# Kernel optimization log

Measured on AMD Instinct MI355X. Metric: run time of the kernel, lower is better.

Reference implementation:

```python
import jax, jax.numpy as jnp
import numpy as np

EPS = 1e-12  # matches torch F.normalize eps


def _l2n(x, axis):
    return x / jnp.maximum(jnp.linalg.norm(x, axis=axis, keepdims=True), EPS)


def setup_inputs() -> dict:
    key = jax.random.key(0)
    k1, k2, k3 = jax.random.split(key, 3)
    x = jax.random.normal(k1, (4, 128, 30, 40), dtype=jnp.float32)
    conv_w = jax.random.normal(k2, (64, 128), dtype=jnp.float32) * 0.02  # 1x1 conv, no bias (vladv2=False)
    centroids = jax.random.uniform(k3, (64, 128), dtype=jnp.float32)
    return {"x": x, "conv_w": conv_w, "centroids": centroids}


def reference(x, conv_w, centroids):
    N, C, H, W = x.shape
    K = centroids.shape[0]
    ps, stride = 4, 1  # patch_sizes='4', strides='1'

    # descriptor-wise L2 normalization of input
    x = _l2n(x, 1)

    # 1x1 conv + softmax over clusters -> soft assignment [N,K,H,W]
    soft_assign = jax.nn.softmax(jnp.einsum('kc,nchw->nkhw', conv_w, x), axis=1)

    # weighted residuals [N,K,C,H,W] (vectorized form of the per-cluster loop)
    res = (x[:, None] - centroids[None, :, :, None, None]) * soft_assign[:, :, None]

    # global VLAD: sum over spatial, intra-norm, flatten, L2-norm
    vlad_global = res.sum(axis=(-1, -2))            # [N,K,C]
    vlad_global = _l2n(vlad_global, 2).reshape(N, K * C)
    vlad_global = _l2n(vlad_global, 1)

    # integral image over spatial dims with zero pad on top/left
    r = res.reshape(N, K * C, H, W)
    integ = jnp.cumsum(jnp.cumsum(r, axis=-1), axis=-2)
    integ = jnp.pad(integ, ((0, 0), (0, 0), (1, 0), (1, 0)))  # [N,KC,H+1,W+1]

    # dilated 2x2 box-filter conv == 4-corner integral-image lookup
    TL = integ[:, :, :H + 1 - ps:stride, :W + 1 - ps:stride]
    TR = integ[:, :, :H + 1 - ps:stride, ps::stride]
    BL = integ[:, :, ps::stride, :W + 1 - ps:stride]
    BR = integ[:, :, ps::stride, ps::stride]
    vl = (TL - TR - BL + BR) / (ps * ps)            # [N,KC,Hp,Wp]
    Hp, Wp = vl.shape[-2], vl.shape[-1]

    # local VLAD: intra-norm over descriptor dim, then global L2 per patch
    vl = vl.reshape(N, K, C, Hp * Wp)
    vl = _l2n(vl, 2).reshape(N, K * C, Hp * Wp)
    vlad_local = _l2n(vl, 1)

    return vlad_global, vlad_local
```

## Files before the change

### kernel.cpp

```cpp
#include <hip/hip_runtime.h>
#include <math.h>

#define EPSV 1e-12f

namespace {
constexpr int N_  = 4;
constexpr int C_  = 128;
constexpr int H_  = 30;
constexpr int W_  = 40;
constexpr int K_  = 64;
constexpr int HW_ = H_ * W_;
constexpr int HP_ = 27;
constexpr int WP_ = 37;
constexpr int P_  = HP_ * WP_;
constexpr int PS_ = 1000;
constexpr int KC_ = K_ * C_;
constexpr int CP_ = C_ * P_;
constexpr int CS_ = HP_ * W_;
constexpr int SL_ = CS_ / 4;
constexpr int CVP_ = 132;
}

static __device__ __forceinline__ float4 ld4(const float* p) {
    return *reinterpret_cast<const float4*>(p);
}
static __device__ __forceinline__ float dot4(float4 a, float4 b) {
    return a.x * b.x + a.y * b.y + a.z * b.z + a.w * b.w;
}
static __device__ __forceinline__ float4 f4add(float4 a, float4 b) {
    return make_float4(a.x + b.x, a.y + b.y, a.z + b.z, a.w + b.w);
}

__global__ __launch_bounds__(256) void k1_norm_softmax(
    const float* __restrict__ x, const float* __restrict__ conv_w,
    float* __restrict__ xnT, float* __restrict__ xnP, float* __restrict__ sa)
{
    __shared__ float xrow[C_ * W_];
    __shared__ float conv_s[K_ * CVP_];
    __shared__ float xrowT[W_ * CVP_];
    __shared__ float invn[W_];
    __shared__ float s_s[K_ * W_];

    const int b = blockIdx.x;
    const int n = b / H_, h = b - n * H_;
    const int t = threadIdx.x;

    for (int i = t; i < C_ * W_; i += 256) {
        const int c = i / W_, w = i - c * W_;
        xrow[i] = x[(size_t)(n * C_ + c) * HW_ + h * W_ + w];
    }
    for (int i = t; i < K_ * C_; i += 256) {
        const int k = i >> 7, c = i & 127;
        conv_s[k * CVP_ + c] = conv_w[i];
    }
    __syncthreads();

    if (t < W_) {
        float s = 0.f;
        for (int c = 0; c < C_; ++c) { const float v = xrow[c * W_ + t]; s += v * v; }
        invn[t] = 1.f / fmaxf(sqrtf(s), EPSV);
    }
    __syncthreads();

    for (int i = t; i < C_ * W_; i += 256) {
        const int c = i / W_, w = i - c * W_;
        const float v = xrow[i] * invn[w];
        xrow[i] = v;
        xnT[(size_t)(n * C_ + c) * HW_ + h * W_ + w] = v;
    }
    __syncthreads();

    for (int i = t; i < W_ * C_; i += 256) {
        const int w = i / C_, c = i - w * C_;
        const float v = xrow[c * W_ + w];
        xnP[((size_t)n * HW_ + h * W_ + w) * C_ + c] = v;
        xrowT[w * CVP_ + c] = v;
    }
    __syncthreads();

    {
        const int k = t >> 2, q = t & 3;
        float acc0 = 0.f, acc1 = 0.f, acc2 = 0.f, acc3 = 0.f, acc4 = 0.f;
        float acc5 = 0.f, acc6 = 0.f, acc7 = 0.f, acc8 = 0.f, acc9 = 0.f;
        const float* convk = &conv_s[k * CVP_];
        for (int ch = 0; ch < 4; ++ch) {
            float4 cv0 = ld4(convk + ch * 32 + 0),  cv1 = ld4(convk + ch * 32 + 4);
            float4 cv2 = ld4(convk + ch * 32 + 8),  cv3 = ld4(convk + ch * 32 + 12);
            float4 cv4 = ld4(convk + ch * 32 + 16), cv5 = ld4(convk + ch * 32 + 20);
            float4 cv6 = ld4(convk + ch * 32 + 24), cv7 = ld4(convk + ch * 32 + 28);
#pragma unroll
            for (int wi = 0; wi < 10; ++wi) {
                const float* xw = &xrowT[(q * 10 + wi) * CVP_ + ch * 32];
                float s = dot4(cv0, ld4(xw)) + dot4(cv1, ld4(xw + 4))
                        + dot4(cv2, ld4(xw + 8)) + dot4(cv3, ld4(xw + 12))
                        + dot4(cv4, ld4(xw + 16)) + dot4(cv5, ld4(xw + 20))
                        + dot4(cv6, ld4(xw + 24)) + dot4(cv7, ld4(xw + 28));
                if      (wi == 0) acc0 += s; else if (wi == 1) acc1 += s;
                else if (wi == 2) acc2 += s; else if (wi == 3) acc3 += s;
                else if (wi == 4) acc4 += s; else if (wi == 5) acc5 += s;
                else if (wi == 6) acc6 += s; else if (wi == 7) acc7 += s;
                else if (wi == 8) acc8 += s; else              acc9 += s;
            }
        }
        float* sd = &s_s[k * W_ + q * 10];
        sd[0] = acc0; sd[1] = acc1; sd[2] = acc2; sd[3] = acc3; sd[4] = acc4;
        sd[5] = acc5; sd[6] = acc6; sd[7] = acc7; sd[8] = acc8; sd[9] = acc9;
    }
    __syncthreads();

    if (t < W_) {
        const int w = t;
        float m = -1e30f;
        for (int k = 0; k < K_; ++k) m = fmaxf(m, s_s[k * W_ + w]);
        float sum = 0.f;
        for (int k = 0; k < K_; ++k) sum += expf(s_s[k * W_ + w] - m);
        const float inv = 1.f / sum;
        for (int k = 0; k < K_; ++k)
            sa[(size_t)(n * K_ + k) * HW_ + h * W_ + w] = expf(s_s[k * W_ + w] - m) * inv;
    }
}

#define COLSUM_VEC_T(cs_q, sa_s, x0, x1, x2, x3)                                \
    for (int s = t; s < SL_; s += 256) {                                        \
        const int i = s * 4;                                                    \
        const float4 sa0 = ld4(&sa_s[i]);                                       \
        const float4 sa1 = ld4(&sa_s[i + W_]);                                  \
        const float4 sa2 = ld4(&sa_s[i + 2 * W_]);                              \
        const float4 sa3 = ld4(&sa_s[i + 3 * W_]);                              \
        float acc[4][4];                                                        \
        const float* xc[4] = {x0, x1, x2, x3};                                  \
        _Pragma("unroll")                                                       \
        for (int ch = 0; ch < 4; ++ch) {                                        \
            const float4 a0 = ld4(xc[ch] + i);                                  \
            const float4 a1 = ld4(xc[ch] + i + W_);                             \
            const float4 a2 = ld4(xc[ch] + i + 2 * W_);                         \
            const float4 a3 = ld4(xc[ch] + i + 3 * W_);                         \
            acc[0][ch] = sa0.x * a0.x + sa1.x * a1.x + sa2.x * a2.x + sa3.x * a3.x; \
            acc[1][ch] = sa0.y * a0.y + sa1.y * a1.y + sa2.y * a2.y + sa3.y * a3.y; \
            acc[2][ch] = sa0.z * a0.z + sa1.z * a1.z + sa2.z * a2.z + sa3.z * a3.z; \
            acc[3][ch] = sa0.w * a0.w + sa1.w * a1.w + sa2.w * a2.w + sa3.w * a3.w; \
        }                                                                       \
        _Pragma("unroll")                                                       \
        for (int q = 0; q < 4; ++q)                                             \
            cs_q[q][s] = make_float4(acc[q][0], acc[q][1], acc[q][2], acc[q][3]); \
    }

#define WINDOW10(cs_q, b0, d, A0, A1, A2, A3)                                   \
    {                                                                           \
        float4 v0 = cs_q[(b0 + 0) & 3][(b0 + 0) >> 2];                          \
        float4 v1 = cs_q[(b0 + 1) & 3][(b0 + 1) >> 2];                          \
        float4 v2 = cs_q[(b0 + 2) & 3][(b0 + 2) >> 2];                          \
        float4 v3 = cs_q[(b0 + 3) & 3][(b0 + 3) >> 2];                          \
        float4 v4 = cs_q[(b0 + 4) & 3][(b0 + 4) >> 2];                          \
        float4 v5 = cs_q[(b0 + 5) & 3][(b0 + 5) >> 2];                          \
        float4 v6 = cs_q[(b0 + 6) & 3][(b0 + 6) >> 2];                          \
        float4 v7 = cs_q[(b0 + 7) & 3][(b0 + 7) >> 2];                          \
        float4 v8 = cs_q[(b0 + 8) & 3][(b0 + 8) >> 2];                          \
        float4 v9 = cs_q[(b0 + 9) & 3][(b0 + 9) >> 2];                          \
        const float4 t0 = f4add(v0, v1), t1 = f4add(v1, v2), t2 = f4add(v2, v3);\
        const float4 t3 = f4add(v3, v4), t4 = f4add(v4, v5), t5 = f4add(v5, v6);\
        const float4 t6 = f4add(v6, v7), t7 = f4add(v7, v8), t8 = f4add(v8, v9);\
        const float4 w0 = f4add(t0, t2), w1 = f4add(t1, t3), w2 = f4add(t2, t4);\
        const float4 w3 = f4add(t3, t5), w4 = f4add(t4, t6), w5 = f4add(t5, t7);\
        const float4 w6 = f4add(t6, t8);                                        \
        A0 = (0 < d) ? w0 : w3;                                                 \
        A1 = (1 < d) ? w1 : w4;                                                 \
        A2 = (2 < d) ? w2 : w5;                                                 \
        A3 = (3 < d) ? w3 : w6;                                                 \
    }

__global__ __launch_bounds__(256) void k4_merged(
    const float* __restrict__ sa, const float* __restrict__ xnT,
    const float* __restrict__ xnP, const float* __restrict__ cent,
    float* __restrict__ nsqp, float* __restrict__ vg_u,
    float* __restrict__ vg_r)
{
    __shared__ float  sa_s[HW_ + 8];
    __shared__ float4 cs_q[4][SL_ + 1];
    __shared__ float  gs[256], bss[256];
    __shared__ float  red[2];

    const int t = threadIdx.x;

    if (blockIdx.x < 256) {
        const int b = blockIdx.x;
        const int n = b >> 6, k = b & 63;
        const int c = t & 127, half = t >> 7;
        constexpr int HHW = HW_ / 2;

        const float* sarow = &sa[(size_t)b * HW_ + half * HHW];
        const float* xp = &xnP[((size_t)n * HW_ + half * HHW) * C_ + c];
        float g0 = 0.f, g1 = 0.f, g2 = 0.f, g3 = 0.f;
        float b0 = 0.f, b1 = 0.f, b2 = 0.f, b3 = 0.f;
        for (int pix = 0; pix < HHW; pix += 4) {
            const float s0 = sarow[pix + 0], s1 = sarow[pix + 1];
            const float s2 = sarow[pix + 2], s3 = sarow[pix + 3];
            g0 += s0 * xp[(size_t)(pix + 0) * C_];
            g1 += s1 * xp[(size_t)(pix + 1) * C_];
            g2 += s2 * xp[(size_t)(pix + 2) * C_];
            g3 += s3 * xp[(size_t)(pix + 3) * C_];
            b0 += s0; b1 += s1; b2 += s2; b3 += s3;
        }
        gs[t]  = (g0 + g1) + (g2 + g3);
        bss[t] = (b0 + b1) + (b2 + b3);
        __syncthreads();

        float vg = 0.f;
        if (t < 128) {
            vg = (gs[t] + gs[t + 128]) - cent[k * C_ + c] * (bss[t] + bss[t + 128]);
            float nsq = vg * vg;
            for (int off = 32; off >= 1; off >>= 1) nsq += __shfl_down(nsq, off);
            if ((t & 63) == 0) red[t >> 6] = nsq;
        }
        __syncthreads();
        const float tot  = red[0] + red[1];
        const float norm = sqrtf(tot);
        const float iv   = 1.f / fmaxf(norm, EPSV);
        if (t < 128) vg_u[(size_t)b * C_ + t] = vg * iv;
        if (t == 0) { const float rr = norm * iv; vg_r[b] = rr * rr; }
        return;
    }

    const int b  = blockIdx.x - 256;
    const int cq = b & 3;
    const int nk = b >> 2;
    const int n  = nk >> 6, k = nk & 63;

    for (int i = t; i < HW_; i += 256) sa_s[i] = sa[(size_t)nk * HW_ + i];
    __syncthreads();

    int hp0 = 0, b0 = 0, d = 4;
    float B0 = 0.f, B1 = 0.f, B2 = 0.f, B3 = 0.f;
    if (t < 250) {
        const int p0 = 4 * t;
        hp0 = p0 / WP_;
        const int wp0 = p0 - hp0 * WP_;
        b0 = p0 + 3 * hp0;
        d  = WP_ - wp0;
        const float* r0 = &sa_s[hp0 * W_ + wp0];
        float sc[10];
#pragma unroll
        for (int j = 0; j < 10; ++j)
            sc[j] = r0[j] + r0[j + W_] + r0[j + 2 * W_] + r0[j + 3 * W_];
        const float u0 = sc[0] + sc[1], u1 = sc[1] + sc[2], u2 = sc[2] + sc[3];
        const float u3 = sc[3] + sc[4], u4 = sc[4] + sc[5], u5 = sc[5] + sc[6];
        const float u6 = sc[6] + sc[7], u7 = sc[7] + sc[8], u8 = sc[8] + sc[9];
        const float wB0 = u0 + u2, wB1 = u1 + u3, wB2 = u2 + u4;
        const float wB3 = u3 + u5, wB4 = u4 + u6, wB5 = u5 + u7, wB6 = u6 + u8;
        B0 = (0 < d) ? wB0 : wB3;
        B1 = (1 < d) ? wB1 : wB4;
        B2 = (2 < d) ? wB2 : wB5;
        B3 = (3 < d) ? wB3 : wB6;
    }

    float4 nv0 = make_float4(0, 0, 0, 0), nv1 = nv0, nv2 = nv0, nv3 = nv0;
    const float* xb = xnT + (size_t)n * C_ * HW_;

    for (int g = 0; g < 8; ++g) {
        const int c0 = cq * 32 + g * 4;
        const float* x0 = xb + (size_t)(c0 + 0) * HW_;
        const float* x1 = xb + (size_t)(c0 + 1) * HW_;
        const float* x2 = xb + (size_t)(c0 + 2) * HW_;
        const float* x3 = xb + (size_t)(c0 + 3) * HW_;
        __syncthreads();
        COLSUM_VEC_T(cs_q, sa_s, x0, x1, x2, x3)
        __syncthreads();
        if (t < 250) {
            const float4 ce = ld4(&cent[k * C_ + c0]);
            float4 A0, A1, A2, A3;
            WINDOW10(cs_q, b0, d, A0, A1, A2, A3)
            const float4 e0 = make_float4(A0.x - ce.x * B0, A0.y - ce.y * B0,
                                          A0.z - ce.z * B0, A0.w - ce.w * B0);
            const float4 e1 = make_float4(A1.x - ce.x * B1, A1.y - ce.y * B1,
                                          A1.z - ce.z * B1, A1.w - ce.w * B1);
            const float4 e2 = make_float4(A2.x - ce.x * B2, A2.y - ce.y * B2,
                                          A2.z - ce.z * B2, A2.w - ce.w * B2);
            const float4 e3 = make_float4(A3.x - ce.x * B3, A3.y - ce.y * B3,
                                          A3.z - ce.z * B3, A3.w - ce.w * B3);
            nv0 = make_float4(nv0.x + e0.x * e0.x, nv0.y + e0.y * e0.y,
                              nv0.z + e0.z * e0.z, nv0.w + e0.w * e0.w);
            nv1 = make_float4(nv1.x + e1.x * e1.x, nv1.y + e1.y * e1.y,
                              nv1.z + e1.z * e1.z, nv1.w + e1.w * e1.w);
            nv2 = make_float4(nv2.x + e2.x * e2.x, nv2.y + e2.y * e2.y,
                              nv2.z + e2.z * e2.z, nv2.w + e2.w * e2.w);
            nv3 = make_float4(nv3.x + e3.x * e3.x, nv3.y + e3.y * e3.y,
                              nv3.z + e3.z * e3.z, nv3.w + e3.w * e3.w);
        }
    }
    if (t < 250) {
        const float s0 = (nv0.x + nv0.y) + (nv0.z + nv0.w);
        const float s1 = (nv1.x + nv1.y) + (nv1.z + nv1.w);
        const float s2 = (nv2.x + nv2.y) + (nv2.z + nv2.w);
        const float s3 = (nv3.x + nv3.y) + (nv3.z + nv3.w);
        *reinterpret_cast<float4*>(&nsqp[(size_t)b * PS_ + 4 * t]) =
            make_float4(s0 * 0.00390625f, s1 * 0.00390625f,
                        s2 * 0.00390625f, s3 * 0.00390625f);
    }
}

__global__ __launch_bounds__(256) void k5_merged(
    const float* __restrict__ nsqp, float* __restrict__ inv1,
    float* __restrict__ rloc, const float* __restrict__ vg_u,
    const float* __restrict__ vg_r, float* __restrict__ out)
{
    const int t = threadIdx.x;
    if (blockIdx.x >= 256) {
        const int n = blockIdx.x - 256;
        __shared__ float inv2s;
        if (t == 0) {
            float s = 0.f;
            for (int k = 0; k < K_; ++k) s += vg_r[n * K_ + k];
            inv2s = 1.f / fmaxf(sqrtf(s), EPSV);
        }
        __syncthreads();
        const float inv2 = inv2s;
        for (int i = t; i < KC_; i += 256)
            out[(size_t)n * KC_ + i] = vg_u[(size_t)n * KC_ + i] * inv2;
        return;
    }
    const int nk = blockIdx.x;
    if (t < 250) {
        const int p0 = 4 * t;
        const float4 a = ld4(&nsqp[(size_t)(nk * 4 + 0) * PS_ + p0]);
        const float4 b = ld4(&nsqp[(size_t)(nk * 4 + 1) * PS_ + p0]);
        const float4 c = ld4(&nsqp[(size_t)(nk * 4 + 2) * PS_ + p0]);
        const float4 e = ld4(&nsqp[(size_t)(nk * 4 + 3) * PS_ + p0]);
        float4 iv, rr;
#pragma unroll
        for (int j = 0; j < 4; ++j) {
            const float s = reinterpret_cast<const float*>(&a)[j]
                          + reinterpret_cast<const float*>(&b)[j]
                          + reinterpret_cast<const float*>(&c)[j]
                          + reinterpret_cast<const float*>(&e)[j];
            const float norm = sqrtf(s);
            const float v = 1.f / fmaxf(norm, EPSV);
            reinterpret_cast<float*>(&iv)[j] = v * 0.0625f;
            const float r = norm * v;
            reinterpret_cast<float*>(&rr)[j] = r * r;
        }
        *reinterpret_cast<float4*>(&inv1[(size_t)nk * PS_ + p0]) = iv;
        *reinterpret_cast<float4*>(&rloc[(size_t)nk * PS_ + p0]) = rr;
    }
}

__global__ __launch_bounds__(256) void k6_inv2(
    const float* __restrict__ rloc, float* __restrict__ inv2)
{
    const int n = blockIdx.x;
    const int t = threadIdx.x;
    if (t < 250) {
        const int p0 = 4 * t;
        float4 s = make_float4(0, 0, 0, 0);
        for (int k = 0; k < K_; ++k) {
            const float4 r = ld4(&rloc[(size_t)(n * K_ + k) * PS_ + p0]);
            s = f4add(s, r);
        }
        float4 o;
        o.x = 1.f / fmaxf(sqrtf(s.x), EPSV);
        o.y = 1.f / fmaxf(sqrtf(s.y), EPSV);
        o.z = 1.f / fmaxf(sqrtf(s.z), EPSV);
        o.w = 1.f / fmaxf(sqrtf(s.w), EPSV);
        *reinterpret_cast<float4*>(&inv2[n * PS_ + p0]) = o;
    }
}

__global__ __launch_bounds__(256) void k7_write(
    const float* __restrict__ sa, const float* __restrict__ xnT,
    const float* __restrict__ cent, const float* __restrict__ inv1,
    const float* __restrict__ inv2, float* __restrict__ outl)
{
    __shared__ float  sa_s[HW_ + 8];
    __shared__ float  scl_s[P_];
    __shared__ float  t2_s[P_];
    __shared__ float4 cs_q[4][SL_ + 1];

    const int b  = blockIdx.x;
    const int cq = b & 3;
    const int nk = b >> 2;
    const int n  = nk >> 6, k = nk & 63;
    const int t  = threadIdx.x;

    for (int i = t; i < HW_; i += 256) sa_s[i] = sa[(size_t)nk * HW_ + i];
    __syncthreads();
    for (int p = t; p < P_; p += 256) {
        const int hp = p / WP_, wp = p - hp * WP_;
        float bs = 0.f;
#pragma unroll
        for (int dh = 0; dh < 4; ++dh) {
            const float* r = &sa_s[(hp + dh) * W_ + wp];
            bs += r[0] + r[1] + r[2] + r[3];
        }
        const float sc = inv1[(size_t)nk * PS_ + p] * inv2[n * PS_ + p];
        scl_s[p] = sc;
        t2_s[p]  = bs * sc;
    }

    const float* xb = xnT + (size_t)n * C_ * HW_;
    float* ob = outl + (size_t)nk * CP_;

    for (int g = 0; g < 8; ++g) {
        const int m = g & 3, h8 = g >> 2;
        const int c0 = cq * 32 + h8 * 16 + m;
        const float* x0 = xb + (size_t)(c0 + 0) * HW_;
        const float* x1 = xb + (size_t)(c0 + 4) * HW_;
        const float* x2 = xb + (size_t)(c0 + 8) * HW_;
        const float* x3 = xb + (size_t)(c0 + 12) * HW_;
        __syncthreads();
        COLSUM_VEC_T(cs_q, sa_s, x0, x1, x2, x3)
        __syncthreads();
        const float ce0 = cent[k * C_ + c0];
        const float ce1 = cent[k * C_ + c0 + 4];
        const float ce2 = cent[k * C_ + c0 + 8];
        const float ce3 = cent[k * C_ + c0 + 12];
        float* ob0 = ob + (size_t)(c0 + 0) * P_;
        float* ob1 = ob + (size_t)(c0 + 4) * P_;
        float* ob2 = ob + (size_t)(c0 + 8) * P_;
        float* ob3 = ob + (size_t)(c0 + 12) * P_;

        if (t < 249) {
            const int p0 = m + 4 * t;
            const int hp0 = p0 / WP_;
            const int wp0 = p0 - hp0 * WP_;
            const int b0 = p0 + 3 * hp0;
            const int d  = WP_ - wp0;
            const float sc0 = scl_s[p0 + 0], sc1 = scl_s[p0 + 1];
            const float sc2 = scl_s[p0 + 2], sc3 = scl_s[p0 + 3];
            const float tt0 = t2_s[p0 + 0], tt1 = t2_s[p0 + 1];
            const float tt2 = t2_s[p0 + 2], tt3 = t2_s[p0 + 3];
            float4 A0, A1, A2, A3;
            WINDOW10(cs_q, b0, d, A0, A1, A2, A3)
            const float4 s0v = make_float4(A0.x * sc0 - ce0 * tt0, A1.x * sc1 - ce0 * tt1,
                                           A2.x * sc2 - ce0 * tt2, A3.x * sc3 - ce0 * tt3);
            const float4 s1v = make_float4(A0.y * sc0 - ce1 * tt0, A1.y * sc1 - ce1 * tt1,
                                           A2.y * sc2 - ce1 * tt2, A3.y * sc3 - ce1 * tt3);
            const float4 s2v = make_float4(A0.z * sc0 - ce2 * tt0, A1.z * sc1 - ce2 * tt1,
                                           A2.z * sc2 - ce2 * tt2, A3.z * sc3 - ce2 * tt3);
            const float4 s3v = make_float4(A0.w * sc0 - ce3 * tt0, A1.w * sc1 - ce3 * tt1,
                                           A2.w * sc2 - ce3 * tt2, A3.w * sc3 - ce3 * tt3);
            *reinterpret_cast<float4*>(ob0 + p0) = s0v;
            *reinterpret_cast<float4*>(ob1 + p0) = s1v;
            *reinterpret_cast<float4*>(ob2 + p0) = s2v;
            *reinterpret_cast<float4*>(ob3 + p0) = s3v;
        } else if (t < 252) {
            const int u = t - 249;
            const int p = (u < m) ? u : 996 + u;
            const int hp = p / WP_, wp = p - hp * WP_;
            const int base = hp * W_ + wp;
            const float4 s0 = cs_q[(base + 0) & 3][(base + 0) >> 2];
            const float4 s1 = cs_q[(base + 1) & 3][(base + 1) >> 2];
            const float4 s2 = cs_q[(base + 2) & 3][(base + 2) >> 2];
            const float4 s3 = cs_q[(base + 3) & 3][(base + 3) >> 2];
            const float sc = scl_s[p], tt = t2_s[p];
            ob0[p] = (s0.x + s1.x + s2.x + s3.x) * sc - ce0 * tt;
            ob1[p] = (s0.y + s1.y + s2.y + s3.y) * sc - ce1 * tt;
            ob2[p] = (s0.z + s1.z + s2.z + s3.z) * sc - ce2 * tt;
            ob3[p] = (s0.w + s1.w + s2.w + s3.w) * sc - ce3 * tt;
        }
    }
}

extern "C" void kernel_launch(void* const* d_in, const int* in_sizes, int n_in,
                              void* d_out, int out_size, void* d_ws, size_t ws_size,
                              hipStream_t stream)
{
    const float* x      = (const float*)d_in[0];
    const float* conv_w = (const float*)d_in[1];
    const float* cent   = (const float*)d_in[2];
    float* out = (float*)d_out;
    float* ws  = (float*)d_ws;

    float* xnT  = ws;
    float* xnP  = ws + 614400;
    float* sa   = ws + 1228800;
    float* vg_u = ws + 1536000;
    float* vg_r = ws + 1568768;
    float* nsqp = ws + 1569024;
    float* inv1 = ws + 2593024;
    float* rloc = ws + 2849024;
    float* inv2 = ws + 3105024;

    float* outl = out + (size_t)N_ * KC_;

    k1_norm_softmax<<<N_ * H_, 256, 0, stream>>>(x, conv_w, xnT, xnP, sa);
    k4_merged<<<256 + N_ * K_ * 4, 256, 0, stream>>>(sa, xnT, xnP, cent,
                                                     nsqp, vg_u, vg_r);
    k5_merged<<<256 + N_, 256, 0, stream>>>(nsqp, inv1, rloc, vg_u, vg_r, out);
    k6_inv2<<<N_, 256, 0, stream>>>(rloc, inv2);
    k7_write<<<N_ * K_ * 4, 256, 0, stream>>>(sa, xnT, cent, inv1, inv2, outl);
}
```

Measured before the change: 120.2 us.

## Compute column sums with vertical strip reuse and process 8 channels per pass

Replaces the per-row 4-tap column-sum loop with a strip scheme. Each thread loads 7 rows of a 4-wide column once and forms four overlapping vertical 4-sums, so loaded rows and softmax weights are reused instead of reloaded. The column-sum buffer is doubled so each iteration handles 8 channels instead of 4, halving the number of barrier-separated passes in both the norm and output kernels. The cost is that only 140 of 256 threads compute column sums, register pressure rises from the 28 float4 partials, and shared memory use grows.

New measurement: 118.9 us. No clear change (-1.0%).

```diff
diff --git a/kernel.cpp b/kernel.cpp
--- a/kernel.cpp
+++ b/kernel.cpp
@@ -29,6 +29,9 @@
 }
 static __device__ __forceinline__ float4 f4add(float4 a, float4 b) {
     return make_float4(a.x + b.x, a.y + b.y, a.z + b.z, a.w + b.w);
+}
+static __device__ __forceinline__ float4 f4mul(float4 a, float4 b) {
+    return make_float4(a.x * b.x, a.y * b.y, a.z * b.z, a.w * b.w);
 }
 
 __global__ __launch_bounds__(256) void k1_norm_softmax(
@@ -120,43 +123,55 @@
     }
 }
 
-#define COLSUM_VEC_T(cs_q, sa_s, x0, x1, x2, x3)                                \
-    for (int s = t; s < SL_; s += 256) {                                        \
-        const int i = s * 4;                                                    \
-        const float4 sa0 = ld4(&sa_s[i]);                                       \
-        const float4 sa1 = ld4(&sa_s[i + W_]);                                  \
-        const float4 sa2 = ld4(&sa_s[i + 2 * W_]);                              \
-        const float4 sa3 = ld4(&sa_s[i + 3 * W_]);                              \
-        float acc[4][4];                                                        \
-        const float* xc[4] = {x0, x1, x2, x3};                                  \
+#define COLSUM_STRIP(cs_q, sa_s, xb, cA_base)                                   \
+    if (t < 140) {                                                              \
+        const int q2 = t / 70, item = t - q2 * 70;                              \
+        const int hq = item / 10, wq = item - hq * 10;                          \
+        const int h0 = 4 * hq;                                                  \
+        const int nh = (hq < 6) ? 4 : 3;                                        \
+        const int cA = (cA_base) + q2 * 16;                                     \
+        const float* xp0 = xb + (size_t)(cA + 0)  * HW_ + h0 * W_ + 4 * wq;     \
+        const float* xp1 = xb + (size_t)(cA + 4)  * HW_ + h0 * W_ + 4 * wq;     \
+        const float* xp2 = xb + (size_t)(cA + 8)  * HW_ + h0 * W_ + 4 * wq;     \
+        const float* xp3 = xb + (size_t)(cA + 12) * HW_ + h0 * W_ + 4 * wq;     \
+        const float* sap = &sa_s[h0 * W_ + 4 * wq];                             \
+        float4 p0[7], p1[7], p2[7], p3[7];                                      \
         _Pragma("unroll")                                                       \
-        for (int ch = 0; ch < 4; ++ch) {                                        \
-            const float4 a0 = ld4(xc[ch] + i);                                  \
-            const float4 a1 = ld4(xc[ch] + i + W_);                             \
-            const float4 a2 = ld4(xc[ch] + i + 2 * W_);                         \
-            const float4 a3 = ld4(xc[ch] + i + 3 * W_);                         \
-            acc[0][ch] = sa0.x * a0.x + sa1.x * a1.x + sa2.x * a2.x + sa3.x * a3.x; \
-            acc[1][ch] = sa0.y * a0.y + sa1.y * a1.y + sa2.y * a2.y + sa3.y * a3.y; \
-            acc[2][ch] = sa0.z * a0.z + sa1.z * a1.z + sa2.z * a2.z + sa3.z * a3.z; \
-            acc[3][ch] = sa0.w * a0.w + sa1.w * a1.w + sa2.w * a2.w + sa3.w * a3.w; \
+        for (int r = 0; r < 7; ++r) {                                           \
+            const float4 sv = ld4(sap + r * W_);                                \
+            p0[r] = f4mul(sv, ld4(xp0 + r * W_));                               \
+            p1[r] = f4mul(sv, ld4(xp1 + r * W_));                               \
+            p2[r] = f4mul(sv, ld4(xp2 + r * W_));                               \
+            p3[r] = f4mul(sv, ld4(xp3 + r * W_));                               \
         }                                                                       \
         _Pragma("unroll")                                                       \
-        for (int q = 0; q < 4; ++q)                                             \
-            cs_q[q][s] = make_float4(acc[q][0], acc[q][1], acc[q][2], acc[q][3]); \
-    }
-
-#define WINDOW10(cs_q, b0, d, A0, A1, A2, A3)                                   \
+        for (int hh = 0; hh < 4; ++hh) {                                        \
+            if (hh < nh) {                                                      \
+                const float4 c0v = f4add(f4add(p0[hh], p0[hh+1]), f4add(p0[hh+2], p0[hh+3])); \
+                const float4 c1v = f4add(f4add(p1[hh], p1[hh+1]), f4add(p1[hh+2], p1[hh+3])); \
+                const float4 c2v = f4add(f4add(p2[hh], p2[hh+1]), f4add(p2[hh+2], p2[hh+3])); \
+                const float4 c3v = f4add(f4add(p3[hh], p3[hh+1]), f4add(p3[hh+2], p3[hh+3])); \
+                const int s = 10 * (h0 + hh) + wq;                              \
+                cs_q[q2][0][s] = make_float4(c0v.x, c1v.x, c2v.x, c3v.x);       \
+                cs_q[q2][1][s] = make_float4(c0v.y, c1v.y, c2v.y, c3v.y);       \
+                cs_q[q2][2][s] = make_float4(c0v.z, c1v.z, c2v.z, c3v.z);       \
+                cs_q[q2][3][s] = make_float4(c0v.w, c1v.w, c2v.w, c3v.w);       \
+            }                                                                   \
+        }                                                                       \
+    }
+
+#define WINDOW10(csq, b0, d, A0, A1, A2, A3)                                    \
     {                                                                           \
-        float4 v0 = cs_q[(b0 + 0) & 3][(b0 + 0) >> 2];                          \
-        float4 v1 = cs_q[(b0 + 1) & 3][(b0 + 1) >> 2];                          \
-        float4 v2 = cs_q[(b0 + 2) & 3][(b0 + 2) >> 2];                          \
-        float4 v3 = cs_q[(b0 + 3) & 3][(b0 + 3) >> 2];                          \
-        float4 v4 = cs_q[(b0 + 4) & 3][(b0 + 4) >> 2];                          \
-        float4 v5 = cs_q[(b0 + 5) & 3][(b0 + 5) >> 2];                          \
-        float4 v6 = cs_q[(b0 + 6) & 3][(b0 + 6) >> 2];                          \
-        float4 v7 = cs_q[(b0 + 7) & 3][(b0 + 7) >> 2];                          \
-        float4 v8 = cs_q[(b0 + 8) & 3][(b0 + 8) >> 2];                          \
-        float4 v9 = cs_q[(b0 + 9) & 3][(b0 + 9) >> 2];                          \
+        float4 v0 = csq[(b0 + 0) & 3][(b0 + 0) >> 2];                           \
+        float4 v1 = csq[(b0 + 1) & 3][(b0 + 1) >> 2];                           \
+        float4 v2 = csq[(b0 + 2) & 3][(b0 + 2) >> 2];                           \
+        float4 v3 = csq[(b0 + 3) & 3][(b0 + 3) >> 2];                           \
+        float4 v4 = csq[(b0 + 4) & 3][(b0 + 4) >> 2];                           \
+        float4 v5 = csq[(b0 + 5) & 3][(b0 + 5) >> 2];                           \
+        float4 v6 = csq[(b0 + 6) & 3][(b0 + 6) >> 2];                           \
+        float4 v7 = csq[(b0 + 7) & 3][(b0 + 7) >> 2];                           \
+        float4 v8 = csq[(b0 + 8) & 3][(b0 + 8) >> 2];                           \
+        float4 v9 = csq[(b0 + 9) & 3][(b0 + 9) >> 2];                           \
         const float4 t0 = f4add(v0, v1), t1 = f4add(v1, v2), t2 = f4add(v2, v3);\
         const float4 t3 = f4add(v3, v4), t4 = f4add(v4, v5), t5 = f4add(v5, v6);\
         const float4 t6 = f4add(v6, v7), t7 = f4add(v7, v8), t8 = f4add(v8, v9);\
@@ -175,8 +190,8 @@
     float* __restrict__ nsqp, float* __restrict__ vg_u,
     float* __restrict__ vg_r)
 {
-    __shared__ float  sa_s[HW_ + 8];
-    __shared__ float4 cs_q[4][SL_ + 1];
+    __shared__ float  sa_s[1248];
+    __shared__ float4 cs_q[2][4][SL_ + 1];
     __shared__ float  gs[256], bss[256];
     __shared__ float  red[2];
 
@@ -229,11 +244,11 @@
     for (int i = t; i < HW_; i += 256) sa_s[i] = sa[(size_t)nk * HW_ + i];
     __syncthreads();
 
-    int hp0 = 0, b0 = 0, d = 4;
-    float B0 = 0.f, B1 = 0.f, B2 = 0.f, B3 = 0.f;
+    int b0 = 0, d = 4;
+    float Bw0 = 0.f, Bw1 = 0.f, Bw2 = 0.f, Bw3 = 0.f;
     if (t < 250) {
         const int p0 = 4 * t;
-        hp0 = p0 / WP_;
+        const int hp0 = p0 / WP_;
         const int wp0 = p0 - hp0 * WP_;
         b0 = p0 + 3 * hp0;
         d  = WP_ - wp0;
@@ -247,54 +262,61 @@
         const float u6 = sc[6] + sc[7], u7 = sc[7] + sc[8], u8 = sc[8] + sc[9];
         const float wB0 = u0 + u2, wB1 = u1 + u3, wB2 = u2 + u4;
         const float wB3 = u3 + u5, wB4 = u4 + u6, wB5 = u5 + u7, wB6 = u6 + u8;
-        B0 = (0 < d) ? wB0 : wB3;
-        B1 = (1 < d) ? wB1 : wB4;
-        B2 = (2 < d) ? wB2 : wB5;
-        B3 = (3 < d) ? wB3 : wB6;
-    }
-
-    float4 nv0 = make_float4(0, 0, 0, 0), nv1 = nv0, nv2 = nv0, nv3 = nv0;
+        Bw0 = (0 < d) ? wB0 : wB3;
+        Bw1 = (1 < d) ? wB1 : wB4;
+        Bw2 = (2 < d) ? wB2 : wB5;
+        Bw3 = (3 < d) ? wB3 : wB6;
+    }
+
+    float nsq0 = 0.f, nsq1 = 0.f, nsq2 = 0.f, nsq3 = 0.f;
     const float* xb = xnT + (size_t)n * C_ * HW_;
 
-    for (int g = 0; g < 8; ++g) {
-        const int c0 = cq * 32 + g * 4;
-        const float* x0 = xb + (size_t)(c0 + 0) * HW_;
-        const float* x1 = xb + (size_t)(c0 + 1) * HW_;
-        const float* x2 = xb + (size_t)(c0 + 2) * HW_;
-        const float* x3 = xb + (size_t)(c0 + 3) * HW_;
-        __syncthreads();
-        COLSUM_VEC_T(cs_q, sa_s, x0, x1, x2, x3)
+    for (int iter = 0; iter < 4; ++iter) {
+        const int c0 = cq * 32 + iter;
+        __syncthreads();
+        COLSUM_STRIP(cs_q, sa_s, xb, c0)
         __syncthreads();
         if (t < 250) {
-            const float4 ce = ld4(&cent[k * C_ + c0]);
-            float4 A0, A1, A2, A3;
-            WINDOW10(cs_q, b0, d, A0, A1, A2, A3)
-            const float4 e0 = make_float4(A0.x - ce.x * B0, A0.y - ce.y * B0,
-                                          A0.z - ce.z * B0, A0.w - ce.w * B0);
-            const float4 e1 = make_float4(A1.x - ce.x * B1, A1.y - ce.y * B1,
-                                          A1.z - ce.z * B1, A1.w - ce.w * B1);
-            const float4 e2 = make_float4(A2.x - ce.x * B2, A2.y - ce.y * B2,
-                                          A2.z - ce.z * B2, A2.w - ce.w * B2);
-            const float4 e3 = make_float4(A3.x - ce.x * B3, A3.y - ce.y * B3,
-                                          A3.z - ce.z * B3, A3.w - ce.w * B3);
-            nv0 = make_float4(nv0.x + e0.x * e0.x, nv0.y + e0.y * e0.y,
-                              nv0.z + e0.z * e0.z, nv0.w + e0.w * e0.w);
-            nv1 = make_float4(nv1.x + e1.x * e1.x, nv1.y + e1.y * e1.y,
-                              nv1.z + e1.z * e1.z, nv1.w + e1.w * e1.w);
-            nv2 = make_float4(nv2.x + e2.x * e2.x, nv2.y + e2.y * e2.y,
-                              nv2.z + e2.z * e2.z, nv2.w + e2.w * e2.w);
-            nv3 = make_float4(nv3.x + e3.x * e3.x, nv3.y + e3.y * e3.y,
-                              nv3.z + e3.z * e3.z, nv3.w + e3.w * e3.w);
+            const float* ck = &cent[k * C_ + c0];
+            const float4 ceA = make_float4(ck[0], ck[4], ck[8], ck[12]);
+            const float4 ceB = make_float4(ck[16], ck[20], ck[24], ck[28]);
+            float4 A0, A1, A2, A3, Q0, Q1, Q2, Q3;
+            WINDOW10(cs_q[0], b0, d, A0, A1, A2, A3)
+            WINDOW10(cs_q[1], b0, d, Q0, Q1, Q2, Q3)
+            {
+                const float4 e = make_float4(A0.x - ceA.x * Bw0, A0.y - ceA.y * Bw0,
+                                             A0.z - ceA.z * Bw0, A0.w - ceA.w * Bw0);
+                const float4 f = make_float4(Q0.x - ceB.x * Bw0, Q0.y - ceB.y * Bw0,
+                                             Q0.z - ceB.z * Bw0, Q0.w - ceB.w * Bw0);
+                nsq0 += dot4(e, e) + dot4(f, f);
+            }
+            {
+                const float4 e = make_float4(A1.x - ceA.x * Bw1, A1.y - ceA.y * Bw1,
+                                             A1.z - ceA.z * Bw1, A1.w - ceA.w * Bw1);
+                const float4 f = make_float4(Q1.x - ceB.x * Bw1, Q1.y - ceB.y * Bw1,
+                                             Q1.z - ceB.z * Bw1, Q1.w - ceB.w * Bw1);
+                nsq1 += dot4(e, e) + dot4(f, f);
+            }
+            {
+                const float4 e = make_float4(A2.x - ceA.x * Bw2, A2.y - ceA.y * Bw2,
+                                             A2.z - ceA.z * Bw2, A2.w - ceA.w * Bw2);
+                const float4 f = make_float4(Q2.x - ceB.x * Bw2, Q2.y - ceB.y * Bw2,
+                                             Q2.z - ceB.z * Bw2, Q2.w - ceB.w * Bw2);
+                nsq2 += dot4(e, e) + dot4(f, f);
+            }
+            {
+                const float4 e = make_float4(A3.x - ceA.x * Bw3, A3.y - ceA.y * Bw3,
+                                             A3.z - ceA.z * Bw3, A3.w - ceA.w * Bw3);
+                const float4 f = make_float4(Q3.x - ceB.x * Bw3, Q3.y - ceB.y * Bw3,
+                                             Q3.z - ceB.z * Bw3, Q3.w - ceB.w * Bw3);
+                nsq3 += dot4(e, e) + dot4(f, f);
+            }
         }
     }
     if (t < 250) {
-        const float s0 = (nv0.x + nv0.y) + (nv0.z + nv0.w);
-        const float s1 = (nv1.x + nv1.y) + (nv1.z + nv1.w);
-        const float s2 = (nv2.x + nv2.y) + (nv2.z + nv2.w);
-        const float s3 = (nv3.x + nv3.y) + (nv3.z + nv3.w);
         *reinterpret_cast<float4*>(&nsqp[(size_t)b * PS_ + 4 * t]) =
-            make_float4(s0 * 0.00390625f, s1 * 0.00390625f,
-                        s2 * 0.00390625f, s3 * 0.00390625f);
+            make_float4(nsq0 * 0.00390625f, nsq1 * 0.00390625f,
+                        nsq2 * 0.00390625f, nsq3 * 0.00390625f);
     }
 }
 
@@ -369,10 +391,10 @@
     const float* __restrict__ cent, const float* __restrict__ inv1,
     const float* __restrict__ inv2, float* __restrict__ outl)
 {
-    __shared__ float  sa_s[HW_ + 8];
+    __shared__ float  sa_s[1248];
     __shared__ float  scl_s[P_];
     __shared__ float  t2_s[P_];
-    __shared__ float4 cs_q[4][SL_ + 1];
+    __shared__ float4 cs_q[2][4][SL_ + 1];
 
     const int b  = blockIdx.x;
     const int cq = b & 3;
@@ -398,24 +420,23 @@
     const float* xb = xnT + (size_t)n * C_ * HW_;
     float* ob = outl + (size_t)nk * CP_;
 
-    for (int g = 0; g < 8; ++g) {
-        const int m = g & 3, h8 = g >> 2;
-        const int c0 = cq * 32 + h8 * 16 + m;
-        const float* x0 = xb + (size_t)(c0 + 0) * HW_;
-        const float* x1 = xb + (size_t)(c0 + 4) * HW_;
-        const float* x2 = xb + (size_t)(c0 + 8) * HW_;
-        const float* x3 = xb + (size_t)(c0 + 12) * HW_;
-        __syncthreads();
-        COLSUM_VEC_T(cs_q, sa_s, x0, x1, x2, x3)
-        __syncthreads();
-        const float ce0 = cent[k * C_ + c0];
-        const float ce1 = cent[k * C_ + c0 + 4];
-        const float ce2 = cent[k * C_ + c0 + 8];
-        const float ce3 = cent[k * C_ + c0 + 12];
-        float* ob0 = ob + (size_t)(c0 + 0) * P_;
-        float* ob1 = ob + (size_t)(c0 + 4) * P_;
-        float* ob2 = ob + (size_t)(c0 + 8) * P_;
+    for (int iter = 0; iter < 4; ++iter) {
+        const int m = iter;
+        const int c0 = cq * 32 + m;
+        __syncthreads();
+        COLSUM_STRIP(cs_q, sa_s, xb, c0)
+        __syncthreads();
+        const float* ck = &cent[k * C_ + c0];
+        const float ce0 = ck[0],  ce1 = ck[4],  ce2 = ck[8],  ce3 = ck[12];
+        const float ce4 = ck[16], ce5 = ck[20], ce6 = ck[24], ce7 = ck[28];
+        float* ob0 = ob + (size_t)(c0 + 0)  * P_;
+        float* ob1 = ob + (size_t)(c0 + 4)  * P_;
+        float* ob2 = ob + (size_t)(c0 + 8)  * P_;
         float* ob3 = ob + (size_t)(c0 + 12) * P_;
+        float* ob4 = ob + (size_t)(c0 + 16) * P_;
+        float* ob5 = ob + (size_t)(c0 + 20) * P_;
+        float* ob6 = ob + (size_t)(c0 + 24) * P_;
+        float* ob7 = ob + (size_t)(c0 + 28) * P_;
 
         if (t < 249) {
             const int p0 = m + 4 * t;
@@ -427,34 +448,55 @@
             const float sc2 = scl_s[p0 + 2], sc3 = scl_s[p0 + 3];
             const float tt0 = t2_s[p0 + 0], tt1 = t2_s[p0 + 1];
             const float tt2 = t2_s[p0 + 2], tt3 = t2_s[p0 + 3];
-            float4 A0, A1, A2, A3;
-            WINDOW10(cs_q, b0, d, A0, A1, A2, A3)
-            const float4 s0v = make_float4(A0.x * sc0 - ce0 * tt0, A1.x * sc1 - ce0 * tt1,
-                                           A2.x * sc2 - ce0 * tt2, A3.x * sc3 - ce0 * tt3);
-            const float4 s1v = make_float4(A0.y * sc0 - ce1 * tt0, A1.y * sc1 - ce1 * tt1,
-                                           A2.y * sc2 - ce1 * tt2, A3.y * sc3 - ce1 * tt3);
-            const float4 s2v = make_float4(A0.z * sc0 - ce2 * tt0, A1.z * sc1 - ce2 * tt1,
-                                           A2.z * sc2 - ce2 * tt2, A3.z * sc3 - ce2 * tt3);
-            const float4 s3v = make_float4(A0.w * sc0 - ce3 * tt0, A1.w * sc1 - ce3 * tt1,
-                                           A2.w * sc2 - ce3 * tt2, A3.w * sc3 - ce3 * tt3);
-            *reinterpret_cast<float4*>(ob0 + p0) = s0v;
-            *reinterpret_cast<float4*>(ob1 + p0) = s1v;
-            *reinterpret_cast<float4*>(ob2 + p0) = s2v;
-            *reinterpret_cast<float4*>(ob3 + p0) = s3v;
+            float4 A0, A1, A2, A3, Q0, Q1, Q2, Q3;
+            WINDOW10(cs_q[0], b0, d, A0, A1, A2, A3)
+            WINDOW10(cs_q[1], b0, d, Q0, Q1, Q2, Q3)
+            *reinterpret_cast<float4*>(ob0 + p0) =
+                make_float4(A0.x * sc0 - ce0 * tt0, A1.x * sc1 - ce0 * tt1,
+                            A2.x * sc2 - ce0 * tt2, A3.x * sc3 - ce0 * tt3);
+            *reinterpret_cast<float4*>(ob1 + p0) =
+                make_float4(A0.y * sc0 - ce1 * tt0, A1.y * sc1 - ce1 * tt1,
+                            A2.y * sc2 - ce1 * tt2, A3.y * sc3 - ce1 * tt3);
+            *reinterpret_cast<float4*>(ob2 + p0) =
+                make_float4(A0.z * sc0 - ce2 * tt0, A1.z * sc1 - ce2 * tt1,
+                            A2.z * sc2 - ce2 * tt2, A3.z * sc3 - ce2 * tt3);
+            *reinterpret_cast<float4*>(ob3 + p0) =
+                make_float4(A0.w * sc0 - ce3 * tt0, A1.w * sc1 - ce3 * tt1,
+                            A2.w * sc2 - ce3 * tt2, A3.w * sc3 - ce3 * tt3);
+            *reinterpret_cast<float4*>(ob4 + p0) =
+                make_float4(Q0.x * sc0 - ce4 * tt0, Q1.x * sc1 - ce4 * tt1,
+                            Q2.x * sc2 - ce4 * tt2, Q3.x * sc3 - ce4 * tt3);
+            *reinterpret_cast<float4*>(ob5 + p0) =
+                make_float4(Q0.y * sc0 - ce5 * tt0, Q1.y * sc1 - ce5 * tt1,
+                            Q2.y * sc2 - ce5 * tt2, Q3.y * sc3 - ce5 * tt3);
+            *reinterpret_cast<float4*>(ob6 + p0) =
+                make_float4(Q0.z * sc0 - ce6 * tt0, Q1.z * sc1 - ce6 * tt1,
+                            Q2.z * sc2 - ce6 * tt2, Q3.z * sc3 - ce6 * tt3);
+            *reinterpret_cast<float4*>(ob7 + p0) =
+                make_float4(Q0.w * sc0 - ce7 * tt0, Q1.w * sc1 - ce7 * tt1,
+                            Q2.w * sc2 - ce7 * tt2, Q3.w * sc3 - ce7 * tt3);
         } else if (t < 252) {
             const int u = t - 249;
             const int p = (u < m) ? u : 996 + u;
             const int hp = p / WP_, wp = p - hp * WP_;
             const int base = hp * W_ + wp;
-            const float4 s0 = cs_q[(base + 0) & 3][(base + 0) >> 2];
-            const float4 s1 = cs_q[(base + 1) & 3][(base + 1) >> 2];
-            const float4 s2 = cs_q[(base + 2) & 3][(base + 2) >> 2];
-            const float4 s3 = cs_q[(base + 3) & 3][(base + 3) >> 2];
+            const float4 a0 = cs_q[0][(base + 0) & 3][(base + 0) >> 2];
+            const float4 a1 = cs_q[0][(base + 1) & 3][(base + 1) >> 2];
+            const float4 a2 = cs_q[0][(base + 2) & 3][(base + 2) >> 2];
+            const float4 a3 = cs_q[0][(base + 3) & 3][(base + 3) >> 2];
+            const float4 q0 = cs_q[1][(base + 0) & 3][(base + 0) >> 2];
+            const float4 q1 = cs_q[1][(base + 1) & 3][(base + 1) >> 2];
+            const float4 q2 = cs_q[1][(base + 2) & 3][(base + 2) >> 2];
+            const float4 q3 = cs_q[1][(base + 3) & 3][(base + 3) >> 2];
             const float sc = scl_s[p], tt = t2_s[p];
-            ob0[p] = (s0.x + s1.x + s2.x + s3.x) * sc - ce0 * tt;
-            ob1[p] = (s0.y + s1.y + s2.y + s3.y) * sc - ce1 * tt;
-            ob2[p] = (s0.z + s1.z + s2.z + s3.z) * sc - ce2 * tt;
-            ob3[p] = (s0.w + s1.w + s2.w + s3.w) * sc - ce3 * tt;
+            ob0[p] = (a0.x + a1.x + a2.x + a3.x) * sc - ce0 * tt;
+            ob1[p] = (a0.y + a1.y + a2.y + a3.y) * sc - ce1 * tt;
+            ob2[p] = (a0.z + a1.z + a2.z + a3.z) * sc - ce2 * tt;
+            ob3[p] = (a0.w + a1.w + a2.w + a3.w) * sc - ce3 * tt;
+            ob4[p] = (q0.x + q1.x + q2.x + q3.x) * sc - ce4 * tt;
+            ob5[p] = (q0.y + q1.y + q2.y + q3.y) * sc - ce5 * tt;
+            ob6[p] = (q0.z + q1.z + q2.z + q3.z) * sc - ce6 * tt;
+            ob7[p] = (q0.w + q1.w + q2.w + q3.w) * sc - ce7 * tt;
         }
     }
 }
```
